# Kernel tuning notes

Measured on AMD Instinct MI355X. Metric: run time of the kernel, lower is better.

Reference implementation:

```python
import jax, jax.numpy as jnp
import numpy as np
from jax import lax

NUM_HEADS = 8
EPS = 1e-12  # torch F.normalize default eps


def setup_inputs() -> dict:
    key = jax.random.key(0)
    ks = jax.random.split(key, 5)
    b, c, h, w = 8, 128, 128, 128
    return {
        "x_in": jax.random.normal(ks[0], (b, c, h, w), dtype=jnp.float32),
        "illu_fea": jax.random.normal(ks[1], (b, c, h, w), dtype=jnp.float32),
        "w_qkv": jax.random.normal(ks[2], (3 * c, c), dtype=jnp.float32) * 0.05,
        "w_dw": jax.random.normal(ks[3], (3 * c, 1, 3, 3), dtype=jnp.float32) * 0.2,
        "w_proj": jax.random.normal(ks[4], (c, c), dtype=jnp.float32) * 0.05,
        "temperature": jnp.ones((NUM_HEADS, 1, 1), dtype=jnp.float32),
    }


def _l2norm(t):
    # F.normalize(t, dim=-1, p=2): t / max(||t||_2, eps)
    n = jnp.sqrt(jnp.sum(t * t, axis=-1, keepdims=True))
    return t / jnp.maximum(n, EPS)


def reference(x_in, illu_fea, w_qkv, w_dw, w_proj, temperature):
    b, c, h, w = x_in.shape
    dh = c // NUM_HEADS
    # 1x1 conv (pointwise channel GEMM): [b,c,h,w] -> [b,3c,h,w]
    qkv = jnp.einsum("bchw,oc->bohw", x_in, w_qkv)
    # depthwise 3x3 conv, groups = 3c, SAME padding
    qkv = lax.conv_general_dilated(
        qkv, w_dw, window_strides=(1, 1), padding="SAME",
        dimension_numbers=("NCHW", "OIHW", "NCHW"),
        feature_group_count=3 * c,
    )
    q, k, v = jnp.split(qkv, 3, axis=1)
    # b (head dh) h w -> b head dh (h*w)
    rs = lambda t: t.reshape(b, NUM_HEADS, dh, h * w)
    q, k, v = rs(q), rs(k), rs(v)
    v = v * illu_fea.reshape(b, NUM_HEADS, dh, h * w)  # illumination gating
    q = _l2norm(q)
    k = _l2norm(k)
    # channel-wise attention: [b,head,dh,dh], contract over spatial N = h*w
    attn = jnp.einsum("bhcn,bhdn->bhcd", q, k) * temperature
    attn = jax.nn.softmax(attn, axis=-1)
    out = jnp.einsum("bhcd,bhdn->bhcn", attn, v).reshape(b, c, h, w)
    out = jnp.einsum("bchw,oc->bohw", out, w_proj)  # project_out 1x1 conv
    return out
```

## Files before the change

kernel.cpp:

```cpp
#include <hip/hip_runtime.h>
#include <hip/hip_bf16.h>

typedef __attribute__((ext_vector_type(8))) short bf16x8;
typedef __attribute__((ext_vector_type(4))) float f32x4;

__device__ __forceinline__ unsigned short f2b(float f) {
    unsigned int u = __builtin_bit_cast(unsigned int, f);
    u += 0x7FFFu + ((u >> 16) & 1u);
    return (unsigned short)(u >> 16);
}
__device__ __forceinline__ float b2f(unsigned short h) {
    unsigned int u = ((unsigned int)h) << 16;
    return __builtin_bit_cast(float, u);
}

#define OFFB_QKV1 0L
#define OFFB_DWQK 100663296L
#define OFFB_VGT  167772160L
#define OFFB_WBF  201326592L
#define OFFB_G    201424896L
#define OFFB_NQK  201490432L
#define OFFB_ATTN 201498624L
#define OFFB_CTB  201564160L

__global__ __launch_bounds__(256) void prep_w(const float* __restrict__ w,
                                              unsigned short* __restrict__ wbf)
{
    int e = blockIdx.x * 256 + threadIdx.x;
    float4 v = *(const float4*)&w[e * 4];
    unsigned int p0 = (unsigned int)f2b(v.x) | ((unsigned int)f2b(v.y) << 16);
    unsigned int p1 = (unsigned int)f2b(v.z) | ((unsigned int)f2b(v.w) << 16);
    *(uint2*)&wbf[e * 4] = make_uint2(p0, p1);
}

__global__ __launch_bounds__(256) void transpose_cb(const float* __restrict__ in,
                                                    unsigned short* __restrict__ out)
{
    const int b  = blockIdx.z;
    const int c0 = blockIdx.y * 32;
    const int n0 = blockIdx.x * 64;
    __shared__ float s[32][65];
    const int tid = threadIdx.x;
    const float* ib = in + ((long)b * 128 + c0) * 16384 + n0;
#pragma unroll
    for (int i = 0; i < 2; ++i) {
        int e = tid + i * 256;
        int c = e >> 4, n4 = (e & 15) * 4;
        *(float4*)&s[c][n4] = *(const float4*)&ib[(long)c * 16384 + n4];
    }
    __syncthreads();
    const int n = tid >> 2, cg = (tid & 3) * 8;
    unsigned int p[4];
#pragma unroll
    for (int j = 0; j < 4; ++j)
        p[j] = (unsigned int)f2b(s[cg + 2*j][n]) | ((unsigned int)f2b(s[cg + 2*j + 1][n]) << 16);
    *(uint4*)&out[((long)b * 16384 + n0 + n) * 128 + c0 + cg] = make_uint4(p[0], p[1], p[2], p[3]);
}

template<int OUT_BF16>
__global__ __launch_bounds__(256) void mfma_gemm(
    const unsigned short* __restrict__ A, long aBatch,
    const unsigned short* __restrict__ Bt, void* __restrict__ Cv, int M)
{
    const int b  = blockIdx.z;
    const int m0 = blockIdx.y * 128;
    const int n0 = blockIdx.x * 128;
    const unsigned short* Ab = A  + (long)b * aBatch + (long)m0 * 128;
    const unsigned short* Bb = Bt + ((long)b * 16384 + n0) * 128;

    __shared__ unsigned short As[128][136];
    __shared__ unsigned short Bs[128][136];

    const int tid = threadIdx.x;
#pragma unroll
    for (int i = 0; i < 8; ++i) {
        int ch = tid + i * 256;
        int row = ch >> 4, cg = (ch & 15) * 8;
        *(uint4*)&As[row][cg] = *(const uint4*)&Ab[row * 128 + cg];
        *(uint4*)&Bs[row][cg] = *(const uint4*)&Bb[row * 128 + cg];
    }
    __syncthreads();

    const int l  = tid & 63;
    const int w  = tid >> 6;
    const int mb = (w & 1) * 64, nb = (w >> 1) * 64;
    const int lr = l & 15, lg = l >> 4;

    f32x4 acc[4][4];
    const f32x4 zero = {0.f, 0.f, 0.f, 0.f};
#pragma unroll
    for (int mi = 0; mi < 4; ++mi)
#pragma unroll
        for (int ni = 0; ni < 4; ++ni) acc[mi][ni] = zero;

#pragma unroll
    for (int kk = 0; kk < 128; kk += 32) {
        bf16x8 af[4], bfr[4];
#pragma unroll
        for (int mi = 0; mi < 4; ++mi)
            af[mi] = *(const bf16x8*)&As[mb + mi * 16 + lr][kk + lg * 8];
#pragma unroll
        for (int ni = 0; ni < 4; ++ni)
            bfr[ni] = *(const bf16x8*)&Bs[nb + ni * 16 + lr][kk + lg * 8];
#pragma unroll
        for (int mi = 0; mi < 4; ++mi)
#pragma unroll
            for (int ni = 0; ni < 4; ++ni)
                acc[mi][ni] = __builtin_amdgcn_mfma_f32_16x16x32_bf16(
                    af[mi], bfr[ni], acc[mi][ni], 0, 0, 0);
    }

    if (OUT_BF16) {
        __syncthreads();
        unsigned short* ct = &As[0][0];
#pragma unroll
        for (int mi = 0; mi < 4; ++mi)
#pragma unroll
            for (int ni = 0; ni < 4; ++ni)
#pragma unroll
                for (int r = 0; r < 4; ++r)
                    ct[(mb + mi * 16 + lg * 4 + r) * 128 + nb + ni * 16 + lr] =
                        f2b(acc[mi][ni][r]);
        __syncthreads();
        unsigned short* Cg = (unsigned short*)Cv + ((long)b * M + m0) * 16384 + n0;
#pragma unroll
        for (int i = 0; i < 8; ++i) {
            int ch = tid + i * 256;
            int row = ch >> 4, cg = (ch & 15) * 8;
            *(uint4*)&Cg[(long)row * 16384 + cg] = *(const uint4*)&ct[row * 128 + cg];
        }
    } else {
        float* Cg = (float*)Cv + ((long)b * M + m0) * 16384 + n0;
#pragma unroll
        for (int mi = 0; mi < 4; ++mi)
#pragma unroll
            for (int ni = 0; ni < 4; ++ni)
#pragma unroll
                for (int r = 0; r < 4; ++r)
                    Cg[(long)(mb + mi * 16 + lg * 4 + r) * 16384 + nb + ni * 16 + lr] =
                        acc[mi][ni][r];
    }
}

__global__ __launch_bounds__(256) void dw_norm_gate(
    const unsigned short* __restrict__ qkv1, const float* __restrict__ wdw,
    const float* __restrict__ illu, float* __restrict__ Vg,
    unsigned short* __restrict__ dwqk, float* __restrict__ nqk)
{
    const int b = blockIdx.z, ch = blockIdx.y;
    const int y0 = blockIdx.x * 8;
    const int tid = threadIdx.x;
    __shared__ float lds[10][130];
    __shared__ float wsum[4];
    const unsigned short* in = qkv1 + ((long)b * 384 + ch) * 16384;

    float wv[9];
#pragma unroll
    for (int j = 0; j < 9; ++j) wv[j] = wdw[ch * 9 + j];

#pragma unroll
    for (int i = 0; i < 5; ++i) {
        int e = tid + i * 256;
        int row = e >> 7, xx = e & 127;
        int yy = y0 + row - 1;
        lds[row][xx + 1] = (yy >= 0 && yy < 128) ? b2f(in[yy * 128 + xx]) : 0.f;
    }
    if (tid < 10) lds[tid][0] = 0.f;
    else if (tid < 20) lds[tid - 10][129] = 0.f;
    __syncthreads();

    const int x = tid & 127;
    const int rbase = (tid >> 7) * 4;
    float o[4];
#pragma unroll
    for (int rr = 0; rr < 4; ++rr) {
        int ry = rbase + rr;
        float a = 0.f;
#pragma unroll
        for (int ky = 0; ky < 3; ++ky)
#pragma unroll
            for (int kx = 0; kx < 3; ++kx)
                a = fmaf(wv[ky * 3 + kx], lds[ry + ky][x + kx], a);
        o[rr] = a;
    }

    if (ch >= 256) {
        const int c = ch - 256;
        const float* ib = illu + ((long)b * 128 + c) * 16384 + y0 * 128;
        float*       ob = Vg   + ((long)b * 128 + c) * 16384 + y0 * 128;
#pragma unroll
        for (int rr = 0; rr < 4; ++rr) {
            int ry = rbase + rr;
            ob[ry * 128 + x] = o[rr] * ib[ry * 128 + x];
        }
    } else {
        unsigned short* db = dwqk + ((long)b * 256 + ch) * 16384 + y0 * 128;
        float s = 0.f;
#pragma unroll
        for (int rr = 0; rr < 4; ++rr) {
            int ry = rbase + rr;
            unsigned short h = f2b(o[rr]);
            db[ry * 128 + x] = h;
            float f = b2f(h);
            s = fmaf(f, f, s);
        }
#pragma unroll
        for (int off = 32; off > 0; off >>= 1) s += __shfl_down(s, off);
        if ((tid & 63) == 0) wsum[tid >> 6] = s;
        __syncthreads();
        if (tid == 0) atomicAdd(&nqk[b * 256 + ch], wsum[0] + wsum[1] + wsum[2] + wsum[3]);
    }
}

__global__ __launch_bounds__(256) void gram_mfma(const unsigned short* __restrict__ dwqk,
                                                 float* __restrict__ G)
{
    const int hd = blockIdx.y, b = blockIdx.z;
    const int tid = threadIdx.x;
    const int l = tid & 63, w = tid >> 6;
    const int lr = l & 15, lg = l >> 4;
    const unsigned short* qb = dwqk + ((long)b * 256 + hd * 16) * 16384;
    const unsigned short* kb = dwqk + ((long)b * 256 + 128 + hd * 16) * 16384;
    const int n0 = blockIdx.x * 1024 + w * 256;

    f32x4 acc = {0.f, 0.f, 0.f, 0.f};
#pragma unroll
    for (int ks = 0; ks < 8; ++ks) {
        const int n = n0 + ks * 32 + lg * 8;
        bf16x8 a = *(const bf16x8*)&qb[(long)lr * 16384 + n];
        bf16x8 bb = *(const bf16x8*)&kb[(long)lr * 16384 + n];
        acc = __builtin_amdgcn_mfma_f32_16x16x32_bf16(a, bb, acc, 0, 0, 0);
    }

    __shared__ float sg[4][16][16];
#pragma unroll
    for (int r = 0; r < 4; ++r) sg[w][lg * 4 + r][lr] = acc[r];
    __syncthreads();
    const int row = tid >> 4, col = tid & 15;
    float v = sg[0][row][col] + sg[1][row][col] + sg[2][row][col] + sg[3][row][col];
    atomicAdd(&G[(((long)b * 8 + hd) * 16 + row) * 16 + col], v);
}

__global__ void softmax_attn(const float* __restrict__ G, const float* __restrict__ nqk,
                             const float* __restrict__ temp, float* __restrict__ attn)
{
    const int hd = blockIdx.x, b = blockIdx.y;
    const int r = threadIdx.x;
    if (r >= 16) return;
    const float tv = temp[hd];
    const float* g = G + ((long)(b * 8 + hd) * 16 + r) * 16;
    float mq = fmaxf(sqrtf(nqk[b * 256 + hd * 16 + r]), 1e-12f);
    float L[16];
    float mx = -1e30f;
#pragma unroll
    for (int d = 0; d < 16; ++d) {
        float mk = fmaxf(sqrtf(nqk[b * 256 + 128 + hd * 16 + d]), 1e-12f);
        L[d] = g[d] * tv / (mq * mk);
        mx = fmaxf(mx, L[d]);
    }
    float s = 0.f;
#pragma unroll
    for (int d = 0; d < 16; ++d) { L[d] = expf(L[d] - mx); s += L[d]; }
    float inv = 1.f / s;
    float* arow = attn + ((long)(b * 8 + hd) * 16 + r) * 16;
#pragma unroll
    for (int d = 0; d < 16; ++d) arow[d] = L[d] * inv;
}

__global__ __launch_bounds__(256) void compose_kernel(
    const float* __restrict__ wproj, const float* __restrict__ attn,
    unsigned short* __restrict__ CtBo)
{
    const int b = blockIdx.x, tid = threadIdx.x;
#pragma unroll 1
    for (int e = tid; e < 16384; e += 256) {
        const int o = e >> 7, D = e & 127;
        const int hd = D >> 4, d = D & 15;
        const float* ar = attn + (long)(b * 8 + hd) * 256 + d;
        const float* wr = wproj + o * 128 + hd * 16;
        float s = 0.f;
#pragma unroll
        for (int c2 = 0; c2 < 16; ++c2) s = fmaf(wr[c2], ar[c2 * 16], s);
        CtBo[((long)b * 128 + o) * 128 + D] = f2b(s);
    }
}

extern "C" void kernel_launch(void* const* d_in, const int* in_sizes, int n_in,
                              void* d_out, int out_size, void* d_ws, size_t ws_size,
                              hipStream_t stream)
{
    const float* x     = (const float*)d_in[0];
    const float* illu  = (const float*)d_in[1];
    const float* wqkv  = (const float*)d_in[2];
    const float* wdw   = (const float*)d_in[3];
    const float* wproj = (const float*)d_in[4];
    const float* temp  = (const float*)d_in[5];
    float* out = (float*)d_out;
    char*  wsb = (char*)d_ws;

    unsigned short* qkv1 = (unsigned short*)(wsb + OFFB_QKV1);
    unsigned short* dwqk = (unsigned short*)(wsb + OFFB_DWQK);
    unsigned short* xT   = dwqk;
    unsigned short* VgT  = (unsigned short*)(wsb + OFFB_VGT);
    unsigned short* wbf  = (unsigned short*)(wsb + OFFB_WBF);
    float* G    = (float*)(wsb + OFFB_G);
    float* nqk  = (float*)(wsb + OFFB_NQK);
    float* attn = (float*)(wsb + OFFB_ATTN);
    unsigned short* CtBo = (unsigned short*)(wsb + OFFB_CTB);

    hipLaunchKernelGGL(prep_w, dim3(48), dim3(256), 0, stream, wqkv, wbf);
    hipMemsetAsync(G, 0, 73728, stream);
    hipLaunchKernelGGL(transpose_cb, dim3(256, 4, 8), dim3(256), 0, stream, x, xT);
    hipLaunchKernelGGL(HIP_KERNEL_NAME(mfma_gemm<1>), dim3(128, 3, 8), dim3(256), 0, stream,
                       wbf, 0L, xT, (void*)qkv1, 384);
    hipLaunchKernelGGL(dw_norm_gate, dim3(16, 384, 8), dim3(256), 0, stream,
                       qkv1, wdw, illu, out, dwqk, nqk);
    hipLaunchKernelGGL(gram_mfma, dim3(16, 8, 8), dim3(256), 0, stream, dwqk, G);
    hipLaunchKernelGGL(softmax_attn, dim3(8, 8), dim3(64), 0, stream, G, nqk, temp, attn);
    hipLaunchKernelGGL(compose_kernel, dim3(8), dim3(256), 0, stream, wproj, attn, CtBo);
    hipLaunchKernelGGL(transpose_cb, dim3(256, 4, 8), dim3(256), 0, stream, out, VgT);
    hipLaunchKernelGGL(HIP_KERNEL_NAME(mfma_gemm<0>), dim3(128, 1, 8), dim3(256), 0, stream,
                       CtBo, 16384L, VgT, (void*)out, 128);
}
```

Measured before the change: 347.8 us.

## Store gated V as bf16, vectorize depthwise conv loads, enlarge row tiles

```diff
diff --git a/kernel.cpp b/kernel.cpp
--- a/kernel.cpp
+++ b/kernel.cpp
@@ -57,6 +57,34 @@
     *(uint4*)&out[((long)b * 16384 + n0 + n) * 128 + c0 + cg] = make_uint4(p[0], p[1], p[2], p[3]);
 }
 
+__global__ __launch_bounds__(256) void transpose_vg(const unsigned short* __restrict__ in,
+                                                    unsigned short* __restrict__ out)
+{
+    const int b  = blockIdx.z;
+    const int c0 = blockIdx.y * 32;
+    const int n0 = blockIdx.x * 64;
+    __shared__ float s[32][65];
+    const int tid = threadIdx.x;
+    const unsigned short* ib = in + ((long)b * 128 + c0) * 16384 + n0;
+    {
+        int c = tid >> 3, ng = (tid & 7) * 8;
+        uint4 v = *(const uint4*)&ib[(long)c * 16384 + ng];
+        unsigned int uu[4] = {v.x, v.y, v.z, v.w};
+#pragma unroll
+        for (int j = 0; j < 4; ++j) {
+            s[c][ng + 2*j]     = __builtin_bit_cast(float, uu[j] << 16);
+            s[c][ng + 2*j + 1] = __builtin_bit_cast(float, uu[j] & 0xFFFF0000u);
+        }
+    }
+    __syncthreads();
+    const int n = tid >> 2, cg = (tid & 3) * 8;
+    unsigned int p[4];
+#pragma unroll
+    for (int j = 0; j < 4; ++j)
+        p[j] = (unsigned int)f2b(s[cg + 2*j][n]) | ((unsigned int)f2b(s[cg + 2*j + 1][n]) << 16);
+    *(uint4*)&out[((long)b * 16384 + n0 + n) * 128 + c0 + cg] = make_uint4(p[0], p[1], p[2], p[3]);
+}
+
 template<int OUT_BF16>
 __global__ __launch_bounds__(256) void mfma_gemm(
     const unsigned short* __restrict__ A, long aBatch,
@@ -144,13 +172,13 @@
 
 __global__ __launch_bounds__(256) void dw_norm_gate(
     const unsigned short* __restrict__ qkv1, const float* __restrict__ wdw,
-    const float* __restrict__ illu, float* __restrict__ Vg,
+    const float* __restrict__ illu, unsigned short* __restrict__ Vg,
     unsigned short* __restrict__ dwqk, float* __restrict__ nqk)
 {
     const int b = blockIdx.z, ch = blockIdx.y;
-    const int y0 = blockIdx.x * 8;
-    const int tid = threadIdx.x;
-    __shared__ float lds[10][130];
+    const int y0 = blockIdx.x * 16;
+    const int tid = threadIdx.x;
+    __shared__ float lds[18][136];
     __shared__ float wsum[4];
     const unsigned short* in = qkv1 + ((long)b * 384 + ch) * 16384;
 
@@ -159,46 +187,66 @@
     for (int j = 0; j < 9; ++j) wv[j] = wdw[ch * 9 + j];
 
 #pragma unroll
-    for (int i = 0; i < 5; ++i) {
-        int e = tid + i * 256;
-        int row = e >> 7, xx = e & 127;
-        int yy = y0 + row - 1;
-        lds[row][xx + 1] = (yy >= 0 && yy < 128) ? b2f(in[yy * 128 + xx]) : 0.f;
-    }
-    if (tid < 10) lds[tid][0] = 0.f;
-    else if (tid < 20) lds[tid - 10][129] = 0.f;
-    __syncthreads();
-
-    const int x = tid & 127;
-    const int rbase = (tid >> 7) * 4;
-    float o[4];
-#pragma unroll
-    for (int rr = 0; rr < 4; ++rr) {
-        int ry = rbase + rr;
+    for (int i = 0; i < 2; ++i) {
+        int chk = tid + i * 256;
+        if (chk < 288) {
+            int row = chk >> 4, xg = (chk & 15) * 8;
+            int yy = y0 + row - 1;
+            float f[8];
+            if (yy >= 0 && yy < 128) {
+                uint4 v = *(const uint4*)&in[yy * 128 + xg];
+                unsigned int uu[4] = {v.x, v.y, v.z, v.w};
+#pragma unroll
+                for (int j = 0; j < 4; ++j) {
+                    f[2*j]   = __builtin_bit_cast(float, uu[j] << 16);
+                    f[2*j+1] = __builtin_bit_cast(float, uu[j] & 0xFFFF0000u);
+                }
+            } else {
+#pragma unroll
+                for (int j = 0; j < 8; ++j) f[j] = 0.f;
+            }
+            *(float4*)&lds[row][xg + 4] = make_float4(f[0], f[1], f[2], f[3]);
+            *(float4*)&lds[row][xg + 8] = make_float4(f[4], f[5], f[6], f[7]);
+        }
+    }
+    if (tid < 18) lds[tid][3] = 0.f;
+    else if (tid < 50 && tid >= 32) lds[tid - 32][132] = 0.f;
+    __syncthreads();
+
+    const int x  = tid & 127;
+    const int rt = (tid >> 7) * 8;
+    float c0[10], c1[10], c2[10];
+#pragma unroll
+    for (int t = 0; t < 10; ++t) {
+        c0[t] = lds[rt + t][x + 3];
+        c1[t] = lds[rt + t][x + 4];
+        c2[t] = lds[rt + t][x + 5];
+    }
+    float o[8];
+#pragma unroll
+    for (int rr = 0; rr < 8; ++rr) {
         float a = 0.f;
-#pragma unroll
-        for (int ky = 0; ky < 3; ++ky)
-#pragma unroll
-            for (int kx = 0; kx < 3; ++kx)
-                a = fmaf(wv[ky * 3 + kx], lds[ry + ky][x + kx], a);
+        a = fmaf(wv[0], c0[rr],     a); a = fmaf(wv[1], c1[rr],     a); a = fmaf(wv[2], c2[rr],     a);
+        a = fmaf(wv[3], c0[rr + 1], a); a = fmaf(wv[4], c1[rr + 1], a); a = fmaf(wv[5], c2[rr + 1], a);
+        a = fmaf(wv[6], c0[rr + 2], a); a = fmaf(wv[7], c1[rr + 2], a); a = fmaf(wv[8], c2[rr + 2], a);
         o[rr] = a;
     }
 
     if (ch >= 256) {
         const int c = ch - 256;
         const float* ib = illu + ((long)b * 128 + c) * 16384 + y0 * 128;
-        float*       ob = Vg   + ((long)b * 128 + c) * 16384 + y0 * 128;
-#pragma unroll
-        for (int rr = 0; rr < 4; ++rr) {
-            int ry = rbase + rr;
-            ob[ry * 128 + x] = o[rr] * ib[ry * 128 + x];
+        unsigned short* ob = Vg + ((long)b * 128 + c) * 16384 + y0 * 128;
+#pragma unroll
+        for (int rr = 0; rr < 8; ++rr) {
+            int ry = rt + rr;
+            ob[ry * 128 + x] = f2b(o[rr] * ib[ry * 128 + x]);
         }
     } else {
         unsigned short* db = dwqk + ((long)b * 256 + ch) * 16384 + y0 * 128;
         float s = 0.f;
 #pragma unroll
-        for (int rr = 0; rr < 4; ++rr) {
-            int ry = rbase + rr;
+        for (int rr = 0; rr < 8; ++rr) {
+            int ry = rt + rr;
             unsigned short h = f2b(o[rr]);
             db[ry * 128 + x] = h;
             float f = b2f(h);
@@ -307,18 +355,19 @@
     float* nqk  = (float*)(wsb + OFFB_NQK);
     float* attn = (float*)(wsb + OFFB_ATTN);
     unsigned short* CtBo = (unsigned short*)(wsb + OFFB_CTB);
+    unsigned short* Vg   = (unsigned short*)d_out;
 
     hipLaunchKernelGGL(prep_w, dim3(48), dim3(256), 0, stream, wqkv, wbf);
     hipMemsetAsync(G, 0, 73728, stream);
     hipLaunchKernelGGL(transpose_cb, dim3(256, 4, 8), dim3(256), 0, stream, x, xT);
     hipLaunchKernelGGL(HIP_KERNEL_NAME(mfma_gemm<1>), dim3(128, 3, 8), dim3(256), 0, stream,
                        wbf, 0L, xT, (void*)qkv1, 384);
-    hipLaunchKernelGGL(dw_norm_gate, dim3(16, 384, 8), dim3(256), 0, stream,
-                       qkv1, wdw, illu, out, dwqk, nqk);
+    hipLaunchKernelGGL(dw_norm_gate, dim3(8, 384, 8), dim3(256), 0, stream,
+                       qkv1, wdw, illu, Vg, dwqk, nqk);
     hipLaunchKernelGGL(gram_mfma, dim3(16, 8, 8), dim3(256), 0, stream, dwqk, G);
     hipLaunchKernelGGL(softmax_attn, dim3(8, 8), dim3(64), 0, stream, G, nqk, temp, attn);
     hipLaunchKernelGGL(compose_kernel, dim3(8), dim3(256), 0, stream, wproj, attn, CtBo);
-    hipLaunchKernelGGL(transpose_cb, dim3(256, 4, 8), dim3(256), 0, stream, out, VgT);
+    hipLaunchKernelGGL(transpose_vg, dim3(256, 4, 8), dim3(256), 0, stream, Vg, VgT);
     hipLaunchKernelGGL(HIP_KERNEL_NAME(mfma_gemm<0>), dim3(128, 1, 8), dim3(256), 0, stream,
                        CtBo, 16384L, VgT, (void*)out, 128);
 }
```

Measured after the change: 292.6 us. -15.9%, faster.
